# Kernel tuning notes

Measured on AMD Instinct MI355X. Metric: run time of the kernel, lower is better.

## Reference

```python
import jax, jax.numpy as jnp
import numpy as np

BATCH = 4096
DIM = 128
TEMP = 0.5


def setup_inputs() -> dict:
    key = jax.random.key(0)
    k1, k2 = jax.random.split(key)
    z_i = jax.random.normal(k1, (BATCH, DIM), dtype=jnp.float32)
    z_j = jax.random.normal(k2, (BATCH, DIM), dtype=jnp.float32)
    return {"z_i": z_i, "z_j": z_j}


def reference(z_i, z_j):
    # NT-Xent: cosine-sim matrix + masked cross-entropy with positive at column 0.
    n = z_i.shape[0]
    two_n = 2 * n
    z = jnp.concatenate([z_i, z_j], axis=0)                      # [2N, D]
    # cosine similarity via normalize + GEMM (same math as pairwise cosine_similarity)
    zn = z / jnp.linalg.norm(z, axis=-1, keepdims=True)
    sim = (zn @ zn.T) / TEMP                                      # [2N, 2N]
    idx = jnp.arange(two_n)
    # positive pair for row i is column (i+N) mod 2N (== diag(sim, +N) ++ diag(sim, -N))
    pos = sim[idx, (idx + n) % two_n]                             # [2N]
    # cross-entropy with label 0 over logits = [pos, negatives]:
    # the logit set equals all row entries except the self-similarity diagonal,
    # so loss_i = logsumexp_{j != i}(sim[i, j]) - pos_i
    neg_inf = jnp.asarray(-jnp.inf, dtype=sim.dtype)
    sim_masked = jnp.where(idx[:, None] == idx[None, :], neg_inf, sim)
    lse = jax.nn.logsumexp(sim_masked, axis=1)                    # [2N]
    loss = jnp.sum(lse - pos) / two_n
    return loss
```

## Files before the change

### kernel.cpp

```cpp
#include <hip/hip_runtime.h>
#include <hip/hip_bf16.h>

#define NROWS 8192
#define HALFN 4096
#define DIMK  128
#define JC    16
#define LJ    (NROWS / JC)
#define BAND  256
#define NBAND (NROWS / BAND)

typedef __attribute__((ext_vector_type(8))) short short8;
typedef __attribute__((ext_vector_type(4))) float f32x4;

#define EXPSCALE 2.8853900817779268f

static __device__ __forceinline__ float bf2f(unsigned short u) {
    union { float f; unsigned int i; } x;
    x.i = ((unsigned int)u) << 16;
    return x.f;
}

__global__ __launch_bounds__(256) void k_norm(const float* __restrict__ zi,
                                              const float* __restrict__ zj,
                                              unsigned short* __restrict__ znb) {
    const int lane = threadIdx.x & 63;
    const int wave = threadIdx.x >> 6;
    const int row  = blockIdx.x * 4 + wave;
    const float* src = (row < HALFN) ? (zi + (size_t)row * DIMK)
                                     : (zj + (size_t)(row - HALFN) * DIMK);
    float2 v = *reinterpret_cast<const float2*>(src + lane * 2);
    float ss = v.x * v.x + v.y * v.y;
    #pragma unroll
    for (int m = 1; m < 64; m <<= 1) ss += __shfl_xor(ss, m);
    float rn = rsqrtf(ss);
    __hip_bfloat16 ha = __float2bfloat16(v.x * rn);
    __hip_bfloat16 hb = __float2bfloat16(v.y * rn);
    ushort2 o;
    o.x = *reinterpret_cast<unsigned short*>(&ha);
    o.y = *reinterpret_cast<unsigned short*>(&hb);
    *reinterpret_cast<ushort2*>(znb + (size_t)row * DIMK + lane * 2) = o;
}

__global__ __launch_bounds__(256) void k_main(const unsigned short* __restrict__ znb,
                                              float* __restrict__ Spart) {
    const int lane = threadIdx.x & 63;
    const int wave = threadIdx.x >> 6;
    const int band = blockIdx.x & (NBAND - 1);
    const int jc   = blockIdx.x >> 5;
    const int row0 = band * BAND + wave * 64;
    const int jbase = jc * LJ;

    const int rsel = lane & 15;
    const int g    = lane >> 4;

    short8 afr[4][4];
    #pragma unroll
    for (int rf = 0; rf < 4; ++rf)
        #pragma unroll
        for (int kk = 0; kk < 4; ++kk)
            afr[rf][kk] = *reinterpret_cast<const short8*>(
                znb + (size_t)(row0 + rf * 16 + rsel) * DIMK + kk * 32 + g * 8);

    float sacc[4][4];
    #pragma unroll
    for (int rf = 0; rf < 4; ++rf)
        #pragma unroll
        for (int r = 0; r < 4; ++r) sacc[rf][r] = 0.f;

    for (int jt = 0; jt < LJ / 16; ++jt) {
        const int j0 = jbase + jt * 16;
        short8 bfr[4];
        #pragma unroll
        for (int kk = 0; kk < 4; ++kk)
            bfr[kk] = *reinterpret_cast<const short8*>(
                znb + (size_t)(j0 + rsel) * DIMK + kk * 32 + g * 8);

        #pragma unroll
        for (int rf = 0; rf < 4; ++rf) {
            f32x4 c = {0.f, 0.f, 0.f, 0.f};
            #pragma unroll
            for (int kk = 0; kk < 4; ++kk)
                c = __builtin_amdgcn_mfma_f32_16x16x32_bf16(afr[rf][kk], bfr[kk], c, 0, 0, 0);
            const bool isdiag = (j0 == row0 + rf * 16);
            if (__builtin_expect(isdiag, 0)) {
                #pragma unroll
                for (int r = 0; r < 4; ++r) {
                    float e = exp2f(c[r] * EXPSCALE);
                    if (rsel == g * 4 + r) e = 0.f;
                    sacc[rf][r] += e;
                }
            } else {
                #pragma unroll
                for (int r = 0; r < 4; ++r)
                    sacc[rf][r] += exp2f(c[r] * EXPSCALE);
            }
        }
    }

    #pragma unroll
    for (int rf = 0; rf < 4; ++rf)
        #pragma unroll
        for (int r = 0; r < 4; ++r) {
            float v = sacc[rf][r];
            v += __shfl_xor(v, 1);
            v += __shfl_xor(v, 2);
            v += __shfl_xor(v, 4);
            v += __shfl_xor(v, 8);
            sacc[rf][r] = v;
        }
    if (rsel == 0) {
        #pragma unroll
        for (int rf = 0; rf < 4; ++rf) {
            float4 o = make_float4(sacc[rf][0], sacc[rf][1], sacc[rf][2], sacc[rf][3]);
            *reinterpret_cast<float4*>(Spart + (size_t)jc * NROWS + row0 + rf * 16 + g * 4) = o;
        }
    }
}

__global__ __launch_bounds__(256) void k_rowterm(const unsigned short* __restrict__ znb,
                                                 const float* __restrict__ Spart,
                                                 float* __restrict__ terms) {
    const int lane = threadIdx.x & 63;
    const int wave = threadIdx.x >> 6;
    const int row  = blockIdx.x * 4 + wave;
    const int p    = (row + HALFN) & (NROWS - 1);

    ushort2 a = *reinterpret_cast<const ushort2*>(znb + (size_t)row * DIMK + lane * 2);
    ushort2 b = *reinterpret_cast<const ushort2*>(znb + (size_t)p   * DIMK + lane * 2);
    float d = bf2f(a.x) * bf2f(b.x) + bf2f(a.y) * bf2f(b.y);
    float S = (lane < JC) ? Spart[(size_t)lane * NROWS + row] : 0.f;
    #pragma unroll
    for (int m = 1; m < 64; m <<= 1) {
        d += __shfl_xor(d, m);
        S += __shfl_xor(S, m);
    }
    if (lane == 0) terms[row] = __logf(S) - 2.0f * d;
}

__global__ __launch_bounds__(1024) void k_final(const float* __restrict__ terms,
                                                float* __restrict__ out) {
    __shared__ float red[16];
    const int tid = threadIdx.x;
    float s = 0.f;
    for (int k = tid; k < NROWS; k += 1024) s += terms[k];
    #pragma unroll
    for (int m = 1; m < 64; m <<= 1) s += __shfl_xor(s, m);
    if ((tid & 63) == 0) red[tid >> 6] = s;
    __syncthreads();
    if (tid < 64) {
        float v = (tid < 16) ? red[tid] : 0.f;
        #pragma unroll
        for (int m = 1; m < 16; m <<= 1) v += __shfl_xor(v, m);
        if (tid == 0) out[0] = v * (1.0f / (float)NROWS);
    }
}

extern "C" void kernel_launch(void* const* d_in, const int* in_sizes, int n_in,
                              void* d_out, int out_size, void* d_ws, size_t ws_size,
                              hipStream_t stream) {
    const float* zi = (const float*)d_in[0];
    const float* zj = (const float*)d_in[1];
    float* out = (float*)d_out;
    char* ws = (char*)d_ws;

    unsigned short* znb  = (unsigned short*)ws;
    float*         Spart = (float*)(ws + (size_t)NROWS * DIMK * 2);
    float*         terms = (float*)(ws + (size_t)NROWS * DIMK * 2
                                       + (size_t)JC * NROWS * 4);

    k_norm   <<<NROWS / 4, 256, 0, stream>>>(zi, zj, znb);
    k_main   <<<NBAND * JC, 256, 0, stream>>>(znb, Spart);
    k_rowterm<<<NROWS / 4, 256, 0, stream>>>(znb, Spart, terms);
    k_final  <<<1, 1024, 0, stream>>>(terms, out);
}
```

Before: 103.4 us.

## Fold exp scale into normalization, double-buffer B fragments, shrink tiles, reduce per block

The 2/T·log2(e) scale is folded into the normalization as its square root, so the GEMM yields log2-domain logits directly and the per-element multiply before exp2 goes away. The main kernel now processes 32 rows per wave over 32 column chunks, giving 2048 blocks instead of 512, and double-buffers B fragments so the next tile's loads overlap the current MFMA/exp work. The row-term kernel handles 16 rows per block with 16-byte loads and reduces within the block, so the final kernel only sums 512 partials. Trade-offs: smaller A reuse per wave means more B traffic, the extra scale factor is applied before bf16 rounding, and each row's exp sum is now split across 32 partials.

```diff
diff --git a/kernel.cpp b/kernel.cpp
--- a/kernel.cpp
+++ b/kernel.cpp
@@ -4,15 +4,16 @@
 #define NROWS 8192
 #define HALFN 4096
 #define DIMK  128
-#define JC    16
+#define JC    32
 #define LJ    (NROWS / JC)
-#define BAND  256
+#define BAND  128
 #define NBAND (NROWS / BAND)
 
 typedef __attribute__((ext_vector_type(8))) short short8;
 typedef __attribute__((ext_vector_type(4))) float f32x4;
 
-#define EXPSCALE 2.8853900817779268f
+#define SQRT_EXPSCALE 1.6986436f
+#define LN2F          0.69314718f
 
 static __device__ __forceinline__ float bf2f(unsigned short u) {
     union { float f; unsigned int i; } x;
@@ -32,7 +33,7 @@
     float ss = v.x * v.x + v.y * v.y;
     #pragma unroll
     for (int m = 1; m < 64; m <<= 1) ss += __shfl_xor(ss, m);
-    float rn = rsqrtf(ss);
+    float rn = rsqrtf(ss) * SQRT_EXPSCALE;
     __hip_bfloat16 ha = __float2bfloat16(v.x * rn);
     __hip_bfloat16 hb = __float2bfloat16(v.y * rn);
     ushort2 o;
@@ -41,64 +42,78 @@
     *reinterpret_cast<ushort2*>(znb + (size_t)row * DIMK + lane * 2) = o;
 }
 
+#define TILE_COMPUTE(BUF, JT)                                                  \
+    {                                                                          \
+        const int j0 = jbase + (JT) * 16;                                      \
+        _Pragma("unroll")                                                      \
+        for (int rf = 0; rf < 2; ++rf) {                                       \
+            f32x4 c = {0.f, 0.f, 0.f, 0.f};                                    \
+            _Pragma("unroll")                                                  \
+            for (int kk = 0; kk < 4; ++kk)                                     \
+                c = __builtin_amdgcn_mfma_f32_16x16x32_bf16(afr[rf][kk],       \
+                                                            BUF[kk], c, 0, 0, 0); \
+            if (__builtin_expect(j0 == row0 + rf * 16, 0)) {                   \
+                _Pragma("unroll")                                              \
+                for (int r = 0; r < 4; ++r) {                                  \
+                    float e = exp2f(c[r]);                                     \
+                    if (rsel == g * 4 + r) e = 0.f;           \
+                    sacc[rf][r] += e;                                          \
+                }                                                              \
+            } else {                                                           \
+                _Pragma("unroll")                                              \
+                for (int r = 0; r < 4; ++r) sacc[rf][r] += exp2f(c[r]);        \
+            }                                                                  \
+        }                                                                      \
+    }
+
 __global__ __launch_bounds__(256) void k_main(const unsigned short* __restrict__ znb,
                                               float* __restrict__ Spart) {
     const int lane = threadIdx.x & 63;
     const int wave = threadIdx.x >> 6;
     const int band = blockIdx.x & (NBAND - 1);
-    const int jc   = blockIdx.x >> 5;
-    const int row0 = band * BAND + wave * 64;
+    const int jc   = blockIdx.x >> 6;
+    const int row0 = band * BAND + wave * 32;
     const int jbase = jc * LJ;
 
     const int rsel = lane & 15;
     const int g    = lane >> 4;
 
-    short8 afr[4][4];
+    const unsigned short* arow = znb + (size_t)(row0 + rsel) * DIMK + g * 8;
+    short8 afr[2][4];
     #pragma unroll
-    for (int rf = 0; rf < 4; ++rf)
+    for (int rf = 0; rf < 2; ++rf)
         #pragma unroll
         for (int kk = 0; kk < 4; ++kk)
-            afr[rf][kk] = *reinterpret_cast<const short8*>(
-                znb + (size_t)(row0 + rf * 16 + rsel) * DIMK + kk * 32 + g * 8);
+            afr[rf][kk] = *reinterpret_cast<const short8*>(arow + rf * 16 * DIMK + kk * 32);
 
-    float sacc[4][4];
+    float sacc[2][4];
     #pragma unroll
-    for (int rf = 0; rf < 4; ++rf)
+    for (int rf = 0; rf < 2; ++rf)
         #pragma unroll
         for (int r = 0; r < 4; ++r) sacc[rf][r] = 0.f;
 
-    for (int jt = 0; jt < LJ / 16; ++jt) {
-        const int j0 = jbase + jt * 16;
-        short8 bfr[4];
+    const unsigned short* bbase = znb + (size_t)(jbase + rsel) * DIMK + g * 8;
+
+    short8 bA[4], bB[4];
+    #pragma unroll
+    for (int kk = 0; kk < 4; ++kk)
+        bA[kk] = *reinterpret_cast<const short8*>(bbase + kk * 32);
+
+    for (int jt = 0; jt < LJ / 16; jt += 2) {
         #pragma unroll
         for (int kk = 0; kk < 4; ++kk)
-            bfr[kk] = *reinterpret_cast<const short8*>(
-                znb + (size_t)(j0 + rsel) * DIMK + kk * 32 + g * 8);
-
+            bB[kk] = *reinterpret_cast<const short8*>(
+                bbase + (size_t)(jt + 1) * 16 * DIMK + kk * 32);
+        TILE_COMPUTE(bA, jt);
         #pragma unroll
-        for (int rf = 0; rf < 4; ++rf) {
-            f32x4 c = {0.f, 0.f, 0.f, 0.f};
-            #pragma unroll
-            for (int kk = 0; kk < 4; ++kk)
-                c = __builtin_amdgcn_mfma_f32_16x16x32_bf16(afr[rf][kk], bfr[kk], c, 0, 0, 0);
-            const bool isdiag = (j0 == row0 + rf * 16);
-            if (__builtin_expect(isdiag, 0)) {
-                #pragma unroll
-                for (int r = 0; r < 4; ++r) {
-                    float e = exp2f(c[r] * EXPSCALE);
-                    if (rsel == g * 4 + r) e = 0.f;
-                    sacc[rf][r] += e;
-                }
-            } else {
-                #pragma unroll
-                for (int r = 0; r < 4; ++r)
-                    sacc[rf][r] += exp2f(c[r] * EXPSCALE);
-            }
-        }
+        for (int kk = 0; kk < 4; ++kk)
+            bA[kk] = *reinterpret_cast<const short8*>(
+                bbase + (size_t)((jt + 2) & (LJ / 16 - 1)) * 16 * DIMK + kk * 32);
+        TILE_COMPUTE(bB, jt + 1);
     }
 
     #pragma unroll
-    for (int rf = 0; rf < 4; ++rf)
+    for (int rf = 0; rf < 2; ++rf)
         #pragma unroll
         for (int r = 0; r < 4; ++r) {
             float v = sacc[rf][r];
@@ -110,7 +125,7 @@
         }
     if (rsel == 0) {
         #pragma unroll
-        for (int rf = 0; rf < 4; ++rf) {
+        for (int rf = 0; rf < 2; ++rf) {
             float4 o = make_float4(sacc[rf][0], sacc[rf][1], sacc[rf][2], sacc[rf][3]);
             *reinterpret_cast<float4*>(Spart + (size_t)jc * NROWS + row0 + rf * 16 + g * 4) = o;
         }
@@ -119,40 +134,48 @@
 
 __global__ __launch_bounds__(256) void k_rowterm(const unsigned short* __restrict__ znb,
                                                  const float* __restrict__ Spart,
-                                                 float* __restrict__ terms) {
+                                                 float* __restrict__ partial) {
+    __shared__ float red[16];
     const int lane = threadIdx.x & 63;
     const int wave = threadIdx.x >> 6;
-    const int row  = blockIdx.x * 4 + wave;
+    const int rsel = lane & 15;
+    const int g    = lane >> 4;
+    const int row  = blockIdx.x * 16 + wave * 4 + g;
     const int p    = (row + HALFN) & (NROWS - 1);
 
-    ushort2 a = *reinterpret_cast<const ushort2*>(znb + (size_t)row * DIMK + lane * 2);
-    ushort2 b = *reinterpret_cast<const ushort2*>(znb + (size_t)p   * DIMK + lane * 2);
-    float d = bf2f(a.x) * bf2f(b.x) + bf2f(a.y) * bf2f(b.y);
-    float S = (lane < JC) ? Spart[(size_t)lane * NROWS + row] : 0.f;
+    short8 a = *reinterpret_cast<const short8*>(znb + (size_t)row * DIMK + rsel * 8);
+    short8 b = *reinterpret_cast<const short8*>(znb + (size_t)p   * DIMK + rsel * 8);
+    float d = 0.f;
     #pragma unroll
-    for (int m = 1; m < 64; m <<= 1) {
+    for (int i = 0; i < 8; ++i)
+        d += bf2f((unsigned short)a[i]) * bf2f((unsigned short)b[i]);
+    float S = Spart[(size_t)rsel * NROWS + row] + Spart[(size_t)(rsel + 16) * NROWS + row];
+    #pragma unroll
+    for (int m = 1; m < 16; m <<= 1) {
         d += __shfl_xor(d, m);
         S += __shfl_xor(S, m);
     }
-    if (lane == 0) terms[row] = __logf(S) - 2.0f * d;
+    if (rsel == 0) red[wave * 4 + g] = __logf(S) - d * LN2F;
+    __syncthreads();
+    if (threadIdx.x < 16) {
+        float v = red[threadIdx.x];
+        #pragma unroll
+        for (int m = 1; m < 16; m <<= 1) v += __shfl_xor(v, m);
+        if (threadIdx.x == 0) partial[blockIdx.x] = v;
+    }
 }
 
-__global__ __launch_bounds__(1024) void k_final(const float* __restrict__ terms,
-                                                float* __restrict__ out) {
-    __shared__ float red[16];
+__global__ __launch_bounds__(256) void k_final(const float* __restrict__ partial,
+                                               float* __restrict__ out) {
+    __shared__ float red[4];
     const int tid = threadIdx.x;
-    float s = 0.f;
-    for (int k = tid; k < NROWS; k += 1024) s += terms[k];
+    float s = partial[tid] + partial[tid + 256];
     #pragma unroll
     for (int m = 1; m < 64; m <<= 1) s += __shfl_xor(s, m);
     if ((tid & 63) == 0) red[tid >> 6] = s;
     __syncthreads();
-    if (tid < 64) {
-        float v = (tid < 16) ? red[tid] : 0.f;
-        #pragma unroll
-        for (int m = 1; m < 16; m <<= 1) v += __shfl_xor(v, m);
-        if (tid == 0) out[0] = v * (1.0f / (float)NROWS);
-    }
+    if (tid == 0)
+        out[0] = (red[0] + red[1] + red[2] + red[3]) * (1.0f / (float)NROWS);
 }
 
 extern "C" void kernel_launch(void* const* d_in, const int* in_sizes, int n_in,
@@ -163,13 +186,13 @@
     float* out = (float*)d_out;
     char* ws = (char*)d_ws;
 
-    unsigned short* znb  = (unsigned short*)ws;
-    float*         Spart = (float*)(ws + (size_t)NROWS * DIMK * 2);
-    float*         terms = (float*)(ws + (size_t)NROWS * DIMK * 2
-                                       + (size_t)JC * NROWS * 4);
+    unsigned short* znb   = (unsigned short*)ws;
+    float*          Spart = (float*)(ws + (size_t)NROWS * DIMK * 2);
+    float*          part  = (float*)(ws + (size_t)NROWS * DIMK * 2
+                                        + (size_t)JC * NROWS * 4);
 
     k_norm   <<<NROWS / 4, 256, 0, stream>>>(zi, zj, znb);
     k_main   <<<NBAND * JC, 256, 0, stream>>>(znb, Spart);
-    k_rowterm<<<NROWS / 4, 256, 0, stream>>>(znb, Spart, terms);
-    k_final  <<<1, 1024, 0, stream>>>(terms, out);
+    k_rowterm<<<NROWS / 16, 256, 0, stream>>>(znb, Spart, part);
+    k_final  <<<1, 256, 0, stream>>>(part, out);
 }
```

Result: slower. 133.2 us (+28.8%).

## Fold exp scale into normalization, atomically reduce row sums, drop final kernel

Applied to the files above, without the earlier changes.

Scales the normalized bf16 vectors by sqrt(2/(T·ln2)) so the GEMM output feeds exp2 directly without a per-element multiply. The column chunking grows from 16 to 64 blocks per band and the launch bounds add an occupancy hint, giving more parallel blocks. Partial row sums are now combined with atomicAdd into one buffer (zeroed in k_norm), and the per-row term plus final mean are fused into k_rowterm with an atomic add to the output, removing one kernel launch. The cost is extra atomic traffic, nondeterministic float summation order, and a positive-pair dot product rescaled by ln2 from the prescaled values, which adds more bf16 rounding error.

```diff
diff --git a/kernel.cpp b/kernel.cpp
--- a/kernel.cpp
+++ b/kernel.cpp
@@ -4,7 +4,7 @@
 #define NROWS 8192
 #define HALFN 4096
 #define DIMK  128
-#define JC    16
+#define JC    64
 #define LJ    (NROWS / JC)
 #define BAND  256
 #define NBAND (NROWS / BAND)
@@ -12,7 +12,8 @@
 typedef __attribute__((ext_vector_type(8))) short short8;
 typedef __attribute__((ext_vector_type(4))) float f32x4;
 
-#define EXPSCALE 2.8853900817779268f
+#define SQRT_EXPSCALE 1.6986436f
+#define LN2F          0.69314718f
 
 static __device__ __forceinline__ float bf2f(unsigned short u) {
     union { float f; unsigned int i; } x;
@@ -22,7 +23,12 @@
 
 __global__ __launch_bounds__(256) void k_norm(const float* __restrict__ zi,
                                               const float* __restrict__ zj,
-                                              unsigned short* __restrict__ znb) {
+                                              unsigned short* __restrict__ znb,
+                                              float* __restrict__ S,
+                                              float* __restrict__ out) {
+    if (threadIdx.x < 4) S[blockIdx.x * 4 + threadIdx.x] = 0.f;
+    if (blockIdx.x == 0 && threadIdx.x == 0) out[0] = 0.f;
+
     const int lane = threadIdx.x & 63;
     const int wave = threadIdx.x >> 6;
     const int row  = blockIdx.x * 4 + wave;
@@ -32,7 +38,7 @@
     float ss = v.x * v.x + v.y * v.y;
     #pragma unroll
     for (int m = 1; m < 64; m <<= 1) ss += __shfl_xor(ss, m);
-    float rn = rsqrtf(ss);
+    float rn = rsqrtf(ss) * SQRT_EXPSCALE;
     __hip_bfloat16 ha = __float2bfloat16(v.x * rn);
     __hip_bfloat16 hb = __float2bfloat16(v.y * rn);
     ushort2 o;
@@ -41,8 +47,8 @@
     *reinterpret_cast<ushort2*>(znb + (size_t)row * DIMK + lane * 2) = o;
 }
 
-__global__ __launch_bounds__(256) void k_main(const unsigned short* __restrict__ znb,
-                                              float* __restrict__ Spart) {
+__global__ __launch_bounds__(256, 4) void k_main(const unsigned short* __restrict__ znb,
+                                                 float* __restrict__ S) {
     const int lane = threadIdx.x & 63;
     const int wave = threadIdx.x >> 6;
     const int band = blockIdx.x & (NBAND - 1);
@@ -53,13 +59,15 @@
     const int rsel = lane & 15;
     const int g    = lane >> 4;
 
+    const unsigned short* arow = znb + (size_t)(row0 + rsel) * DIMK + g * 8;
     short8 afr[4][4];
     #pragma unroll
     for (int rf = 0; rf < 4; ++rf)
         #pragma unroll
-        for (int kk = 0; kk < 4; ++kk)
-            afr[rf][kk] = *reinterpret_cast<const short8*>(
-                znb + (size_t)(row0 + rf * 16 + rsel) * DIMK + kk * 32 + g * 8);
+        for (int kk = 0; kk < 4; ++kk) {
+            afr[rf][kk] = *reinterpret_cast<const short8*>(arow + rf * 16 * DIMK + kk * 32);
+            asm volatile("" :: "v"(afr[rf][kk]));
+        }
 
     float sacc[4][4];
     #pragma unroll
@@ -67,32 +75,31 @@
         #pragma unroll
         for (int r = 0; r < 4; ++r) sacc[rf][r] = 0.f;
 
+    const unsigned short* bbase = znb + (size_t)(jbase + rsel) * DIMK + g * 8;
+
     for (int jt = 0; jt < LJ / 16; ++jt) {
-        const int j0 = jbase + jt * 16;
         short8 bfr[4];
         #pragma unroll
         for (int kk = 0; kk < 4; ++kk)
             bfr[kk] = *reinterpret_cast<const short8*>(
-                znb + (size_t)(j0 + rsel) * DIMK + kk * 32 + g * 8);
-
+                bbase + (size_t)jt * 16 * DIMK + kk * 32);
+        const int j0 = jbase + jt * 16;
         #pragma unroll
         for (int rf = 0; rf < 4; ++rf) {
             f32x4 c = {0.f, 0.f, 0.f, 0.f};
             #pragma unroll
             for (int kk = 0; kk < 4; ++kk)
                 c = __builtin_amdgcn_mfma_f32_16x16x32_bf16(afr[rf][kk], bfr[kk], c, 0, 0, 0);
-            const bool isdiag = (j0 == row0 + rf * 16);
-            if (__builtin_expect(isdiag, 0)) {
+            if (__builtin_expect(j0 == row0 + rf * 16, 0)) {
                 #pragma unroll
                 for (int r = 0; r < 4; ++r) {
-                    float e = exp2f(c[r] * EXPSCALE);
+                    float e = exp2f(c[r]);
                     if (rsel == g * 4 + r) e = 0.f;
                     sacc[rf][r] += e;
                 }
             } else {
                 #pragma unroll
-                for (int r = 0; r < 4; ++r)
-                    sacc[rf][r] += exp2f(c[r] * EXPSCALE);
+                for (int r = 0; r < 4; ++r) sacc[rf][r] += exp2f(c[r]);
             }
         }
     }
@@ -110,48 +117,39 @@
         }
     if (rsel == 0) {
         #pragma unroll
-        for (int rf = 0; rf < 4; ++rf) {
-            float4 o = make_float4(sacc[rf][0], sacc[rf][1], sacc[rf][2], sacc[rf][3]);
-            *reinterpret_cast<float4*>(Spart + (size_t)jc * NROWS + row0 + rf * 16 + g * 4) = o;
-        }
+        for (int rf = 0; rf < 4; ++rf)
+            #pragma unroll
+            for (int r = 0; r < 4; ++r)
+                atomicAdd(&S[row0 + rf * 16 + g * 4 + r], sacc[rf][r]);
     }
 }
 
 __global__ __launch_bounds__(256) void k_rowterm(const unsigned short* __restrict__ znb,
-                                                 const float* __restrict__ Spart,
-                                                 float* __restrict__ terms) {
+                                                 const float* __restrict__ S,
+                                                 float* __restrict__ out) {
+    __shared__ float red[16];
     const int lane = threadIdx.x & 63;
     const int wave = threadIdx.x >> 6;
-    const int row  = blockIdx.x * 4 + wave;
+    const int rsel = lane & 15;
+    const int g    = lane >> 4;
+    const int row  = blockIdx.x * 16 + wave * 4 + g;
     const int p    = (row + HALFN) & (NROWS - 1);
 
-    ushort2 a = *reinterpret_cast<const ushort2*>(znb + (size_t)row * DIMK + lane * 2);
-    ushort2 b = *reinterpret_cast<const ushort2*>(znb + (size_t)p   * DIMK + lane * 2);
-    float d = bf2f(a.x) * bf2f(b.x) + bf2f(a.y) * bf2f(b.y);
-    float S = (lane < JC) ? Spart[(size_t)lane * NROWS + row] : 0.f;
+    short8 a = *reinterpret_cast<const short8*>(znb + (size_t)row * DIMK + rsel * 8);
+    short8 b = *reinterpret_cast<const short8*>(znb + (size_t)p   * DIMK + rsel * 8);
+    float d = 0.f;
     #pragma unroll
-    for (int m = 1; m < 64; m <<= 1) {
-        d += __shfl_xor(d, m);
-        S += __shfl_xor(S, m);
-    }
-    if (lane == 0) terms[row] = __logf(S) - 2.0f * d;
-}
-
-__global__ __launch_bounds__(1024) void k_final(const float* __restrict__ terms,
-                                                float* __restrict__ out) {
-    __shared__ float red[16];
-    const int tid = threadIdx.x;
-    float s = 0.f;
-    for (int k = tid; k < NROWS; k += 1024) s += terms[k];
+    for (int i = 0; i < 8; ++i)
+        d += bf2f((unsigned short)a[i]) * bf2f((unsigned short)b[i]);
     #pragma unroll
-    for (int m = 1; m < 64; m <<= 1) s += __shfl_xor(s, m);
-    if ((tid & 63) == 0) red[tid >> 6] = s;
+    for (int m = 1; m < 16; m <<= 1) d += __shfl_xor(d, m);
+    if (rsel == 0) red[wave * 4 + g] = __logf(S[row]) - d * LN2F;
     __syncthreads();
-    if (tid < 64) {
-        float v = (tid < 16) ? red[tid] : 0.f;
+    if (threadIdx.x < 16) {
+        float v = red[threadIdx.x];
         #pragma unroll
         for (int m = 1; m < 16; m <<= 1) v += __shfl_xor(v, m);
-        if (tid == 0) out[0] = v * (1.0f / (float)NROWS);
+        if (threadIdx.x == 0) atomicAdd(out, v * (1.0f / (float)NROWS));
     }
 }
 
@@ -163,13 +161,10 @@
     float* out = (float*)d_out;
     char* ws = (char*)d_ws;
 
-    unsigned short* znb  = (unsigned short*)ws;
-    float*         Spart = (float*)(ws + (size_t)NROWS * DIMK * 2);
-    float*         terms = (float*)(ws + (size_t)NROWS * DIMK * 2
-                                       + (size_t)JC * NROWS * 4);
+    unsigned short* znb = (unsigned short*)ws;
+    float*          S   = (float*)(ws + (size_t)NROWS * DIMK * 2);
 
-    k_norm   <<<NROWS / 4, 256, 0, stream>>>(zi, zj, znb);
-    k_main   <<<NBAND * JC, 256, 0, stream>>>(znb, Spart);
-    k_rowterm<<<NROWS / 4, 256, 0, stream>>>(znb, Spart, terms);
-    k_final  <<<1, 1024, 0, stream>>>(terms, out);
+    k_norm   <<<NROWS / 4, 256, 0, stream>>>(zi, zj, znb, S, out);
+    k_main   <<<NBAND * JC, 256, 0, stream>>>(znb, S);
+    k_rowterm<<<NROWS / 16, 256, 0, stream>>>(znb, S, out);
 }
```

After: 146.1 us. 41.3% more time.
